# Kernel tuning notes

Hardware: AMD Instinct MI355X
Metric: run time of the kernel (lower is better)

Reference implementation:

```python
import jax, jax.numpy as jnp
import numpy as np

B, N, C = 2, 2048, 1024
H = 16
D = C // H  # head_dim = 64
HID = 4 * C
EPS = 1e-5


def _layernorm(x, g, b):
    mu = jnp.mean(x, axis=-1, keepdims=True)
    var = jnp.var(x, axis=-1, keepdims=True)
    return (x - mu) * jax.lax.rsqrt(var + EPS) * g + b


def _rope(x):
    # x: (B, H, N, D); interleaved-pair rotation, sin/cos computed in fp32
    half = D // 2
    inv_freq = 1.0 / (10000.0 ** (jnp.arange(half, dtype=jnp.float32) / half))
    pos = jnp.arange(N, dtype=jnp.float32)
    freqs = pos[:, None] * inv_freq[None, :]            # (N, half)
    sin = jnp.sin(freqs).astype(x.dtype)
    cos = jnp.cos(freqs).astype(x.dtype)
    xr = x.reshape(*x.shape[:-1], half, 2)
    x1, x2 = xr[..., 0], xr[..., 1]
    r1 = x1 * cos - x2 * sin
    r2 = x1 * sin + x2 * cos
    return jnp.stack((r1, r2), axis=-1).reshape(x.shape)


def setup_inputs() -> dict:
    key = jax.random.key(0)
    ks = jax.random.split(key, 8)
    s = lambda d: 1.0 / np.sqrt(d)
    return {
        "x": jax.random.normal(ks[0], (B, N, C), jnp.float32),
        "ln1_g": jnp.ones((C,), jnp.float32),
        "ln1_b": jnp.zeros((C,), jnp.float32),
        "W_qkv": jax.random.normal(ks[1], (C, 3 * C), jnp.float32) * s(C),
        "b_qkv": jnp.zeros((3 * C,), jnp.float32),
        "W_proj": jax.random.normal(ks[2], (C, C), jnp.float32) * s(C),
        "b_proj": jnp.zeros((C,), jnp.float32),
        "ln2_g": jnp.ones((C,), jnp.float32),
        "ln2_b": jnp.zeros((C,), jnp.float32),
        "W_fc1": jax.random.normal(ks[3], (C, HID), jnp.float32) * s(C),
        "b_fc1": jnp.zeros((HID,), jnp.float32),
        "W_fc2": jax.random.normal(ks[4], (HID, C), jnp.float32) * s(HID),
        "b_fc2": jnp.zeros((C,), jnp.float32),
    }


def reference(x, ln1_g, ln1_b, W_qkv, b_qkv, W_proj, b_proj,
              ln2_g, ln2_b, W_fc1, b_fc1, W_fc2, b_fc2):
    # --- attention branch ---
    h = _layernorm(x, ln1_g, ln1_b)
    qkv = h @ W_qkv + b_qkv                              # (B, N, 3C)
    qkv = qkv.reshape(B, N, 3, H, D).transpose(2, 0, 3, 1, 4)
    q, k, v = qkv[0], qkv[1], qkv[2]                     # each (B, H, N, D)
    q = _rope(q)
    k = _rope(k)
    scale = D ** -0.5
    attn = jnp.einsum('bhnd,bhmd->bhnm', q, k) * scale
    attn = jax.nn.softmax(attn, axis=-1)
    o = jnp.einsum('bhnm,bhmd->bhnd', attn, v)           # (B, H, N, D)
    o = o.transpose(0, 2, 1, 3).reshape(B, N, C)
    x = x + (o @ W_proj + b_proj)
    # --- MLP branch ---
    h = _layernorm(x, ln2_g, ln2_b)
    h = jax.nn.gelu(h @ W_fc1 + b_fc1, approximate=False)
    x = x + (h @ W_fc2 + b_fc2)
    return x
```

## Files before the change

### kernel.cpp

```cpp
#include <hip/hip_runtime.h>
#include <cstdint>
#include <cstddef>

typedef unsigned short u16;
typedef unsigned int   u32;
typedef __attribute__((ext_vector_type(8))) short v8s;
typedef __attribute__((ext_vector_type(4))) float v4f;

#define B_   2
#define N_   2048
#define C_   1024
#define H_   16
#define D_   64
#define HID_ 4096
#define M_   4096

static __device__ __forceinline__ float b2f(u32 u) {
    union { u32 i; float f; } x; x.i = u << 16; return x.f;
}
static __device__ __forceinline__ u16 f2b(float f) {
    union { float f; u32 i; } x; x.f = f;
    u32 r = (x.i + 0x7fffu + ((x.i >> 16) & 1u)) >> 16;
    return (u16)r;
}
static __device__ __forceinline__ u32 scale2(u32 raw, float s) {
    float lo = b2f(raw & 0xffffu) * s, hi = b2f(raw >> 16) * s;
    return (u32)f2b(lo) | ((u32)f2b(hi) << 16);
}

static __device__ __forceinline__ void gload_lds16(const u16* g, u16* l) {
    __builtin_amdgcn_global_load_lds(
        (const __attribute__((address_space(1))) void*)g,
        (__attribute__((address_space(3))) void*)l,
        16, 0, 0);
}

static __device__ __forceinline__ int2 xcd_swz(int gx, int gy) {
    const int nwg = gx * gy;
    int id = blockIdx.y * gx + blockIdx.x;
    id = (id & 7) * (nwg >> 3) + (id >> 3);
    return make_int2(id % gx, id / gx);
}

__global__ __launch_bounds__(256) void transpose_all(const float* __restrict__ Wqkv,
                                                     const float* __restrict__ Wproj,
                                                     const float* __restrict__ Wfc1,
                                                     const float* __restrict__ Wfc2,
                                                     u16* __restrict__ Oqkv,
                                                     u16* __restrict__ Oproj,
                                                     u16* __restrict__ Ofc1,
                                                     u16* __restrict__ Ofc2) {
    __shared__ float tile[32][33];
    int id = blockIdx.x;
    const float* in; u16* out; int K, N, nx;
    if (id < 3072)      { in = Wqkv;  out = Oqkv;  K = 1024; N = 3072; nx = 96;  }
    else if (id < 4096) { in = Wproj; out = Oproj; K = 1024; N = 1024; nx = 32;  id -= 3072; }
    else if (id < 8192) { in = Wfc1;  out = Ofc1;  K = 1024; N = 4096; nx = 128; id -= 4096; }
    else                { in = Wfc2;  out = Ofc2;  K = 4096; N = 1024; nx = 32;  id -= 8192; }
    const int n0 = (id % nx) * 32, k0 = (id / nx) * 32;
    const int c = threadIdx.x & 31, r8 = threadIdx.x >> 5;
#pragma unroll
    for (int i = 0; i < 4; ++i)
        tile[r8 + i * 8][c] = in[(size_t)(k0 + r8 + i * 8) * N + n0 + c];
    __syncthreads();
#pragma unroll
    for (int i = 0; i < 4; ++i)
        out[(size_t)(n0 + r8 + i * 8) * K + k0 + c] = f2b(tile[c][r8 + i * 8]);
}

__global__ __launch_bounds__(256) void ln_kernel(const float* __restrict__ in,
                                                 const float* __restrict__ g,
                                                 const float* __restrict__ b,
                                                 u16* __restrict__ out) {
    __shared__ float ps[4], psq[4];
    __shared__ float stats[2];
    const int row = blockIdx.x;
    const int t = threadIdx.x;
    float4 v = ((const float4*)in)[(size_t)row * 256 + t];
    float s  = v.x + v.y + v.z + v.w;
    float sq = v.x * v.x + v.y * v.y + v.z * v.z + v.w * v.w;
#pragma unroll
    for (int off = 32; off > 0; off >>= 1) { s += __shfl_down(s, off); sq += __shfl_down(sq, off); }
    if ((t & 63) == 0) { ps[t >> 6] = s; psq[t >> 6] = sq; }
    __syncthreads();
    if (t == 0) {
        float S = ps[0] + ps[1] + ps[2] + ps[3];
        float Q = psq[0] + psq[1] + psq[2] + psq[3];
        float mu  = S * (1.f / 1024.f);
        float var = Q * (1.f / 1024.f) - mu * mu;
        stats[0] = mu; stats[1] = rsqrtf(var + 1e-5f);
    }
    __syncthreads();
    const float mu = stats[0], istd = stats[1];
    float4 gg = ((const float4*)g)[t];
    float4 bb = ((const float4*)b)[t];
    ushort4 o;
    o.x = f2b((v.x - mu) * istd * gg.x + bb.x);
    o.y = f2b((v.y - mu) * istd * gg.y + bb.y);
    o.z = f2b((v.z - mu) * istd * gg.z + bb.z);
    o.w = f2b((v.w - mu) * istd * gg.w + bb.w);
    *(ushort4*)&out[(size_t)row * 1024 + t * 4] = o;
}

__global__ __launch_bounds__(256) void rope_table(float2* __restrict__ tab) {
    const int i = blockIdx.x * 256 + threadIdx.x;
    const int d = i & 31, n = i >> 5;
    float inv = powf(10000.f, -(float)d * (1.f / 32.f));
    float fr = (float)n * inv;
    tab[i] = make_float2(cosf(fr), sinf(fr));
}

template <int EPI, int BM>
__global__ __launch_bounds__(256) void gemm_bt(const u16* __restrict__ A,
                                               const u16* __restrict__ Bt,
                                               const float* __restrict__ bias,
                                               void* __restrict__ outp,
                                               const float* __restrict__ resid,
                                               const float2* __restrict__ tab,
                                               int Ndim, int Kdim) {
    constexpr int NACC = (BM == 128) ? 4 : 2;
    constexpr int AISS = BM / 64;
    __shared__ u16 As[3][BM * 32];
    __shared__ u16 Bs[3][128 * 32];
    const int t = threadIdx.x;
    const int lane = t & 63;
    const int w = t >> 6;
    const int wr = (BM == 128) ? (w >> 1) : 0;
    const int wc = (BM == 128) ? (w & 1) : w;
    const int2 lb = xcd_swz(gridDim.x, gridDim.y);
    const int m0 = lb.y * BM, n0 = lb.x * 128;
    const int hi = lane >> 4, lo = lane & 15;

    auto STAGE = [&](int buf, int kt) {
#pragma unroll
        for (int j = 0; j < AISS; ++j) {
            const int c = (w * AISS + j) * 64 + lane;
            gload_lds16(&A[(size_t)(m0 + (c >> 2)) * Kdim + kt + (c & 3) * 8],
                        &As[buf][(w * AISS + j) * 512]);
        }
#pragma unroll
        for (int j = 0; j < 2; ++j) {
            const int c = (w * 2 + j) * 64 + lane;
            gload_lds16(&Bt[(size_t)(n0 + (c >> 2)) * Kdim + kt + (c & 3) * 8],
                        &Bs[buf][(w * 2 + j) * 512]);
        }
    };

    const v4f vzero = {0.f, 0.f, 0.f, 0.f};
    v4f acc[4][NACC];
#pragma unroll
    for (int i = 0; i < 4; ++i)
#pragma unroll
        for (int j = 0; j < NACC; ++j) acc[i][j] = vzero;

    const int nt = Kdim / 32;
    STAGE(0, 0);
    STAGE(1, 32);
    for (int kt = 0; kt < nt; ++kt) {
        if constexpr (BM == 128) asm volatile("s_waitcnt vmcnt(4)" ::: "memory");
        else                     asm volatile("s_waitcnt vmcnt(3)" ::: "memory");
        __builtin_amdgcn_s_barrier();
        if (kt + 2 < nt) STAGE((kt + 2) % 3, (kt + 2) * 32);
        const int cur = kt % 3;
        v8s av[4], bv[NACC];
#pragma unroll
        for (int mi = 0; mi < 4; ++mi)
            av[mi] = *(const v8s*)&As[cur][(wr * 64 + mi * 16 + lo) * 32 + hi * 8];
#pragma unroll
        for (int ni = 0; ni < NACC; ++ni)
            bv[ni] = *(const v8s*)&Bs[cur][(wc * (NACC * 16) + ni * 16 + lo) * 32 + hi * 8];
#pragma unroll
        for (int mi = 0; mi < 4; ++mi)
#pragma unroll
            for (int ni = 0; ni < NACC; ++ni)
                acc[mi][ni] = __builtin_amdgcn_mfma_f32_16x16x32_bf16(av[mi], bv[ni], acc[mi][ni], 0, 0, 0);
    }

#pragma unroll
    for (int mi = 0; mi < 4; ++mi)
#pragma unroll
        for (int ni = 0; ni < NACC; ++ni) {
            const int col = n0 + wc * (NACC * 16) + ni * 16 + lo;
            const float bsv = bias[col];
#pragma unroll
            for (int r = 0; r < 4; ++r) {
                const int row = m0 + wr * 64 + mi * 16 + hi * 4 + r;
                float vacc = acc[mi][ni][r] + bsv;
                if (EPI == 0) {
                    const float partner = __shfl_xor(vacc, 1);
                    const int s = col >> 10;
                    if (s < 2) {
                        const int d = col & 63;
                        const int n = row & 2047;
                        float2 cs = tab[n * 32 + (d >> 1)];
                        vacc = vacc * cs.x + ((d & 1) ? partner * cs.y : -partner * cs.y);
                    }
                    const int rem = col & 1023, hh = rem >> 6, dd = rem & 63;
                    const int bb = row >> 11, nn = row & 2047;
                    ((u16*)outp)[((((size_t)s * B_ + bb) * H_ + hh) * N_ + nn) * D_ + dd] = f2b(vacc);
                } else if (EPI == 1) {
                    ((float*)outp)[(size_t)row * Ndim + col] = vacc + resid[(size_t)row * Ndim + col];
                } else {
                    const float gv = 0.5f * vacc * (1.f + erff(vacc * 0.70710678118f));
                    ((u16*)outp)[(size_t)row * Ndim + col] = f2b(gv);
                }
            }
        }
}

#define SCL_LOG2E 0.1803368801111244f
#define FIXEDM    12.0f

__global__ __launch_bounds__(256) void attn_mfma(const u16* __restrict__ q,
                                                 const u16* __restrict__ k,
                                                 const u16* __restrict__ v,
                                                 u16* __restrict__ out) {
    __shared__ u16 Ks[64 * 64];
    __shared__ u16 Vt[64 * 64];
    __shared__ u16 Ps[4][32 * 64];

    const int t    = threadIdx.x;
    const int w    = t >> 6;
    const int lane = t & 63;
    const int hi   = lane >> 4;
    const int lo   = lane & 15;
    const int2 lb  = xcd_swz(gridDim.x, gridDim.y);
    const int bh   = lb.y;
    const int r0g  = lb.x * 128 + w * 32;

    const u16* qb = q + (size_t)bh * N_ * D_;
    const u16* kb = k + (size_t)bh * N_ * D_;
    const u16* vb = v + (size_t)bh * N_ * D_;

    v8s qa[2][2];
#pragma unroll
    for (int mi = 0; mi < 2; ++mi)
#pragma unroll
        for (int ks = 0; ks < 2; ++ks) {
            uint4 rq = *(const uint4*)&qb[(size_t)(r0g + mi * 16 + lo) * 64 + ks * 32 + hi * 8];
            u32 qs[4];
            qs[0] = scale2(rq.x, SCL_LOG2E); qs[1] = scale2(rq.y, SCL_LOG2E);
            qs[2] = scale2(rq.z, SCL_LOG2E); qs[3] = scale2(rq.w, SCL_LOG2E);
            qa[mi][ks] = *(v8s*)qs;
        }

    u32 ones4[4] = {0x3F803F80u, 0x3F803F80u, 0x3F803F80u, 0x3F803F80u};
    const v8s ones = *(v8s*)ones4;

    const v4f vzero = {0.f, 0.f, 0.f, 0.f};
    v4f o_acc[2][4];
    v4f l_acc[2];
#pragma unroll
    for (int mi = 0; mi < 2; ++mi) {
        l_acc[mi] = vzero;
#pragma unroll
        for (int ni = 0; ni < 4; ++ni) o_acc[mi][ni] = vzero;
    }

    const int vp = t & 31, vg = t >> 5;
    const int vd0 = vg * 8, vkey = vp * 2;

    for (int kt = 0; kt < N_ / 64; ++kt) {
        __syncthreads();
#pragma unroll
        for (int i = 0; i < 2; ++i) {
            const int chunk = i * 256 + t;
            const int key = chunk >> 3, d0 = (chunk & 7) * 8;
            uint4 raw = *(const uint4*)&kb[(size_t)(kt * 64 + key) * 64 + d0];
            *(uint4*)&Ks[key * 64 + (d0 ^ ((key & 7) << 3))] = raw;
        }
        {
            uint4 r0 = *(const uint4*)&vb[(size_t)(kt * 64 + vkey) * 64 + vd0];
            uint4 r1 = *(const uint4*)&vb[(size_t)(kt * 64 + vkey + 1) * 64 + vd0];
            const u32* a0 = (const u32*)&r0;
            const u32* a1 = (const u32*)&r1;
#pragma unroll
            for (int j = 0; j < 8; ++j) {
                u32 lo16 = (j & 1) ? (a0[j >> 1] >> 16) : (a0[j >> 1] & 0xffffu);
                u32 hi16 = (j & 1) ? (a1[j >> 1] >> 16) : (a1[j >> 1] & 0xffffu);
                u32 val = lo16 | (hi16 << 16);
                *(u32*)&Vt[(vd0 + j) * 64 + (vkey ^ (j << 3))] = val;
            }
        }
        __syncthreads();

        v4f s[2][4];
#pragma unroll
        for (int mi = 0; mi < 2; ++mi)
#pragma unroll
            for (int ni = 0; ni < 4; ++ni) s[mi][ni] = vzero;
        __builtin_amdgcn_s_setprio(1);
#pragma unroll
        for (int ks = 0; ks < 2; ++ks)
#pragma unroll
            for (int ni = 0; ni < 4; ++ni) {
                const int key = lo + 16 * ni;
                v8s bv = *(const v8s*)&Ks[key * 64 + ((ks * 32 + hi * 8) ^ ((key & 7) << 3))];
                s[0][ni] = __builtin_amdgcn_mfma_f32_16x16x32_bf16(qa[0][ks], bv, s[0][ni], 0, 0, 0);
                s[1][ni] = __builtin_amdgcn_mfma_f32_16x16x32_bf16(qa[1][ks], bv, s[1][ni], 0, 0, 0);
            }
        __builtin_amdgcn_s_setprio(0);

#pragma unroll
        for (int mi = 0; mi < 2; ++mi)
#pragma unroll
            for (int ni = 0; ni < 4; ++ni)
#pragma unroll
                for (int r = 0; r < 4; ++r)
                    s[mi][ni][r] = exp2f(s[mi][ni][r] - FIXEDM);

#pragma unroll
        for (int mi = 0; mi < 2; ++mi)
#pragma unroll
            for (int f = 0; f < 4; ++f)
#pragma unroll
                for (int rp = 0; rp < 2; ++rp) {
                    u32 pk;
                    asm("v_cvt_pk_bf16_f32 %0, %1, %2"
                        : "=v"(pk) : "v"(s[mi][f][2 * rp]), "v"(s[mi][f][2 * rp + 1]));
                    const int row0 = mi * 16 + hi * 4 + 2 * rp;
                    const int row1 = row0 + 1;
                    Ps[w][row0 * 64 + ((lo + 16 * f) ^ ((row0 & 7) << 3))] = (u16)pk;
                    Ps[w][row1 * 64 + ((lo + 16 * f) ^ ((row1 & 7) << 3))] = (u16)(pk >> 16);
                }
        v8s pa[2][2];
#pragma unroll
        for (int mi = 0; mi < 2; ++mi)
#pragma unroll
            for (int ks = 0; ks < 2; ++ks) {
                const int row = mi * 16 + lo;
                pa[mi][ks] = *(const v8s*)&Ps[w][row * 64 + ((ks * 32 + hi * 8) ^ ((lo & 7) << 3))];
            }

        __builtin_amdgcn_s_setprio(1);
#pragma unroll
        for (int ks = 0; ks < 2; ++ks) {
#pragma unroll
            for (int ni = 0; ni < 4; ++ni) {
                const int dim = lo + 16 * ni;
                v8s vv = *(const v8s*)&Vt[dim * 64 + ((ks * 32 + hi * 8) ^ ((dim & 7) << 3))];
                o_acc[0][ni] = __builtin_amdgcn_mfma_f32_16x16x32_bf16(pa[0][ks], vv, o_acc[0][ni], 0, 0, 0);
                o_acc[1][ni] = __builtin_amdgcn_mfma_f32_16x16x32_bf16(pa[1][ks], vv, o_acc[1][ni], 0, 0, 0);
            }
            l_acc[0] = __builtin_amdgcn_mfma_f32_16x16x32_bf16(pa[0][ks], ones, l_acc[0], 0, 0, 0);
            l_acc[1] = __builtin_amdgcn_mfma_f32_16x16x32_bf16(pa[1][ks], ones, l_acc[1], 0, 0, 0);
        }
        __builtin_amdgcn_s_setprio(0);
    }

    const int bb = bh >> 4, hh = bh & 15;
#pragma unroll
    for (int mi = 0; mi < 2; ++mi)
#pragma unroll
        for (int r = 0; r < 4; ++r) {
            const float inv = 1.f / l_acc[mi][r];
            const int n = r0g + mi * 16 + hi * 4 + r;
#pragma unroll
            for (int ni = 0; ni < 4; ++ni) {
                out[((size_t)bb * N_ + n) * C_ + hh * D_ + lo + 16 * ni] = f2b(o_acc[mi][ni][r] * inv);
            }
        }
}

extern "C" void kernel_launch(void* const* d_in, const int* in_sizes, int n_in,
                              void* d_out, int out_size, void* d_ws, size_t ws_size,
                              hipStream_t stream) {
    (void)in_sizes; (void)n_in; (void)out_size; (void)ws_size;
    const float* x     = (const float*)d_in[0];
    const float* ln1g  = (const float*)d_in[1];
    const float* ln1b  = (const float*)d_in[2];
    const float* Wqkv  = (const float*)d_in[3];
    const float* bqkv  = (const float*)d_in[4];
    const float* Wproj = (const float*)d_in[5];
    const float* bproj = (const float*)d_in[6];
    const float* ln2g  = (const float*)d_in[7];
    const float* ln2b  = (const float*)d_in[8];
    const float* Wfc1  = (const float*)d_in[9];
    const float* bfc1  = (const float*)d_in[10];
    const float* Wfc2  = (const float*)d_in[11];
    const float* bfc2  = (const float*)d_in[12];
    float* out = (float*)d_out;

    char* base = (char*)d_ws;
    const size_t MB = 1024 * 1024;
    u16* Wtqkv  = (u16*)(base);
    u16* Wtproj = (u16*)(base + 6 * MB);
    u16* Wtfc1  = (u16*)(base + 8 * MB);
    u16* Wtfc2  = (u16*)(base + 16 * MB);
    u16* qkv    = (u16*)(base + 24 * MB);
    u16* a1     = (u16*)(base + 24 * MB);
    u16* h1     = (u16*)(base + 56 * MB);
    u16* oatt   = (u16*)(base + 56 * MB);
    u16* h2     = (u16*)(base + 56 * MB);
    float* x1   = (float*)(base + 64 * MB);
    float2* tab = (float2*)(base + 80 * MB);

    transpose_all<<<12288, 256, 0, stream>>>(Wqkv, Wproj, Wfc1, Wfc2,
                                             Wtqkv, Wtproj, Wtfc1, Wtfc2);
    rope_table<<<N_ * (D_ / 2) / 256, 256, 0, stream>>>(tab);
    ln_kernel<<<M_, 256, 0, stream>>>(x, ln1g, ln1b, h1);
    gemm_bt<0, 128><<<dim3(3 * C_ / 128, M_ / 128), 256, 0, stream>>>(h1, Wtqkv, bqkv, qkv, nullptr, tab, 3 * C_, C_);
    attn_mfma<<<dim3(N_ / 128, B_ * H_), 256, 0, stream>>>(
        qkv, qkv + (size_t)B_ * H_ * N_ * D_, qkv + (size_t)2 * B_ * H_ * N_ * D_, oatt);
    gemm_bt<1, 64><<<dim3(C_ / 128, M_ / 64), 256, 0, stream>>>(oatt, Wtproj, bproj, x1, x, nullptr, C_, C_);
    ln_kernel<<<M_, 256, 0, stream>>>(x1, ln2g, ln2b, h2);
    gemm_bt<2, 128><<<dim3(HID_ / 128, M_ / 128), 256, 0, stream>>>(h2, Wtfc1, bfc1, a1, nullptr, nullptr, HID_, C_);
    gemm_bt<1, 64><<<dim3(C_ / 128, M_ / 64), 256, 0, stream>>>(a1, Wtfc2, bfc2, out, x1, nullptr, C_, HID_);
}
```

Before: 304.1 us.

## Split attention over two key halves with a separate combine kernel

The attention kernel now splits the key sequence into two halves across a doubled grid. Each block writes unnormalized fp32 partial outputs and row sums to workspace, and a new combine kernel adds them and normalizes to bf16. This relies on the fixed-max softmax, which needs no rescaling between halves. The aim is to raise block count and occupancy for attention (512 to 1024 blocks on a large-CU GPU). The cost is extra fp32 global traffic of about 32MB written and read, plus one more kernel launch.

```diff
diff --git a/kernel.cpp b/kernel.cpp
--- a/kernel.cpp
+++ b/kernel.cpp
@@ -214,7 +214,8 @@
 __global__ __launch_bounds__(256) void attn_mfma(const u16* __restrict__ q,
                                                  const u16* __restrict__ k,
                                                  const u16* __restrict__ v,
-                                                 u16* __restrict__ out) {
+                                                 float* __restrict__ opart,
+                                                 float* __restrict__ lpart) {
     __shared__ u16 Ks[64 * 64];
     __shared__ u16 Vt[64 * 64];
     __shared__ u16 Ps[4][32 * 64];
@@ -225,7 +226,8 @@
     const int hi   = lane >> 4;
     const int lo   = lane & 15;
     const int2 lb  = xcd_swz(gridDim.x, gridDim.y);
-    const int bh   = lb.y;
+    const int bh   = lb.y >> 1;
+    const int split = lb.y & 1;
     const int r0g  = lb.x * 128 + w * 32;
 
     const u16* qb = q + (size_t)bh * N_ * D_;
@@ -260,7 +262,8 @@
     const int vp = t & 31, vg = t >> 5;
     const int vd0 = vg * 8, vkey = vp * 2;
 
-    for (int kt = 0; kt < N_ / 64; ++kt) {
+    const int kt0 = split * (N_ / 128);
+    for (int kt = kt0; kt < kt0 + N_ / 128; ++kt) {
         __syncthreads();
 #pragma unroll
         for (int i = 0; i < 2; ++i) {
@@ -353,13 +356,39 @@
     for (int mi = 0; mi < 2; ++mi)
 #pragma unroll
         for (int r = 0; r < 4; ++r) {
-            const float inv = 1.f / l_acc[mi][r];
             const int n = r0g + mi * 16 + hi * 4 + r;
+            if (lo == 0)
+                lpart[((size_t)split * (B_ * H_) + bh) * N_ + n] = l_acc[mi][r];
 #pragma unroll
             for (int ni = 0; ni < 4; ++ni) {
-                out[((size_t)bb * N_ + n) * C_ + hh * D_ + lo + 16 * ni] = f2b(o_acc[mi][ni][r] * inv);
-            }
-        }
+                opart[((size_t)(split * B_ + bb) * N_ + n) * C_ + hh * D_ + lo + 16 * ni] =
+                    o_acc[mi][ni][r];
+            }
+        }
+}
+
+__global__ __launch_bounds__(256) void attn_combine(const float* __restrict__ opart,
+                                                    const float* __restrict__ lpart,
+                                                    u16* __restrict__ out) {
+    const int row = blockIdx.x;
+    const int bb = row >> 11, n = row & 2047;
+    const int t = threadIdx.x;
+    const int c0 = t * 4;
+    const int hh = c0 >> 6;
+    const int bh = bb * H_ + hh;
+    const float l0 = lpart[(size_t)bh * N_ + n];
+    const float l1 = lpart[((size_t)(B_ * H_) + bh) * N_ + n];
+    const float inv = 1.f / (l0 + l1);
+    const size_t off0 = ((size_t)bb * N_ + n) * C_ + c0;
+    const size_t off1 = ((size_t)(B_ + bb) * N_ + n) * C_ + c0;
+    float4 a = *(const float4*)&opart[off0];
+    float4 b4 = *(const float4*)&opart[off1];
+    ushort4 o;
+    o.x = f2b((a.x + b4.x) * inv);
+    o.y = f2b((a.y + b4.y) * inv);
+    o.z = f2b((a.z + b4.z) * inv);
+    o.w = f2b((a.w + b4.w) * inv);
+    *(ushort4*)&out[((size_t)bb * N_ + n) * C_ + c0] = o;
 }
 
 extern "C" void kernel_launch(void* const* d_in, const int* in_sizes, int n_in,
@@ -394,14 +423,17 @@
     u16* h2     = (u16*)(base + 56 * MB);
     float* x1   = (float*)(base + 64 * MB);
     float2* tab = (float2*)(base + 80 * MB);
+    float* opart = (float*)(base + 81 * MB);
+    float* lpart = (float*)(base + 113 * MB);
 
     transpose_all<<<12288, 256, 0, stream>>>(Wqkv, Wproj, Wfc1, Wfc2,
                                              Wtqkv, Wtproj, Wtfc1, Wtfc2);
     rope_table<<<N_ * (D_ / 2) / 256, 256, 0, stream>>>(tab);
     ln_kernel<<<M_, 256, 0, stream>>>(x, ln1g, ln1b, h1);
     gemm_bt<0, 128><<<dim3(3 * C_ / 128, M_ / 128), 256, 0, stream>>>(h1, Wtqkv, bqkv, qkv, nullptr, tab, 3 * C_, C_);
-    attn_mfma<<<dim3(N_ / 128, B_ * H_), 256, 0, stream>>>(
-        qkv, qkv + (size_t)B_ * H_ * N_ * D_, qkv + (size_t)2 * B_ * H_ * N_ * D_, oatt);
+    attn_mfma<<<dim3(N_ / 128, 2 * B_ * H_), 256, 0, stream>>>(
+        qkv, qkv + (size_t)B_ * H_ * N_ * D_, qkv + (size_t)2 * B_ * H_ * N_ * D_, opart, lpart);
+    attn_combine<<<M_, 256, 0, stream>>>(opart, lpart, oatt);
     gemm_bt<1, 64><<<dim3(C_ / 128, M_ / 64), 256, 0, stream>>>(oatt, Wtproj, bproj, x1, x, nullptr, C_, C_);
     ln_kernel<<<M_, 256, 0, stream>>>(x1, ln2g, ln2b, h2);
     gemm_bt<2, 128><<<dim3(HID_ / 128, M_ / 128), 256, 0, stream>>>(h2, Wtfc1, bfc1, a1, nullptr, nullptr, HID_, C_);
```

New measurement: 313.2 us. 3.0% more time.

## Add 256x256-tile 8-wave GEMM with interleaved prefetch for FC1+GELU

Applied to the files above, without the earlier changes.

Replaces the 128x128 FC1 GEMM with a new 512-thread kernel that computes 256x256 output tiles, double-buffering LDS in k-halves and interleaving async global-to-LDS prefetch between MFMA groups with priority raises. Larger tiles raise arithmetic intensity and cut redundant global reads of A and B. The trade-offs are a 16x16 grid of only 256 blocks, which may leave CUs underused, heavy register pressure from 32 accumulators per lane, and a manual vmcnt/barrier schedule that must be exactly right.

```diff
diff --git a/kernel.cpp b/kernel.cpp
--- a/kernel.cpp
+++ b/kernel.cpp
@@ -208,6 +208,121 @@
         }
 }
 
+__global__ __launch_bounds__(512, 2) void gemm256_gelu(const u16* __restrict__ A,
+                                                       const u16* __restrict__ Bt,
+                                                       const float* __restrict__ bias,
+                                                       u16* __restrict__ outp,
+                                                       int Ndim, int Kdim) {
+    __shared__ u16 As[2 * 2 * 256 * 32];
+    __shared__ u16 Bs[2 * 2 * 256 * 32];
+    const int t = threadIdx.x;
+    const int lane = t & 63;
+    const int w = t >> 6;
+    const int wr = w >> 2, wc = w & 3;
+    const int hi = lane >> 4, lo = lane & 15;
+    const int2 lb = xcd_swz(gridDim.x, gridDim.y);
+    const int m0 = lb.y * 256, n0 = lb.x * 256;
+    const int koff = (hi * 8) ^ ((lo & 2) << 3);
+
+    auto STAGEH = [&](u16* lds, const u16* src, int rb, int b, int ks, int kt) {
+#pragma unroll
+        for (int j = 0; j < 2; ++j) {
+            const int c = j * 512 + t;
+            const int row = c >> 2;
+            const int e0 = (c & 3) * 8;
+            gload_lds16(&src[(size_t)(rb + row) * Kdim + kt * 64 + ks * 32 + (e0 ^ ((row & 2) << 3))],
+                        &lds[(b * 2 + ks) * 8192 + c * 8]);
+        }
+    };
+    auto RD = [&](const u16* lds, int b, int ks, int row) -> v8s {
+        return *(const v8s*)&lds[(b * 2 + ks) * 8192 + row * 32 + koff];
+    };
+
+    const v4f vzero = {0.f, 0.f, 0.f, 0.f};
+    v4f acc[8][4];
+#pragma unroll
+    for (int i = 0; i < 8; ++i)
+#pragma unroll
+        for (int j = 0; j < 4; ++j) acc[i][j] = vzero;
+
+    const int nt = Kdim / 64;
+    STAGEH(As, A, m0, 0, 0, 0);
+    STAGEH(Bs, Bt, n0, 0, 0, 0);
+    STAGEH(As, A, m0, 0, 1, 0);
+    STAGEH(Bs, Bt, n0, 0, 1, 0);
+
+    for (int I = 0; I < nt; ++I) {
+        const int b = I & 1, nb = b ^ 1;
+        const bool pf = (I + 1 < nt);
+        v8s av[4], bv[4];
+        asm volatile("s_waitcnt vmcnt(4)" ::: "memory");
+        __builtin_amdgcn_s_barrier();
+#pragma unroll
+        for (int n = 0; n < 4; ++n) bv[n] = RD(Bs, b, 0, wc * 64 + n * 16 + lo);
+#pragma unroll
+        for (int m = 0; m < 4; ++m) av[m] = RD(As, b, 0, wr * 128 + m * 16 + lo);
+        if (pf) STAGEH(As, A, m0, nb, 0, I + 1);
+        __builtin_amdgcn_s_setprio(1);
+#pragma unroll
+        for (int m = 0; m < 4; ++m)
+#pragma unroll
+            for (int n = 0; n < 4; ++n)
+                acc[m][n] = __builtin_amdgcn_mfma_f32_16x16x32_bf16(av[m], bv[n], acc[m][n], 0, 0, 0);
+        __builtin_amdgcn_s_setprio(0);
+        __builtin_amdgcn_s_barrier();
+#pragma unroll
+        for (int m = 0; m < 4; ++m) av[m] = RD(As, b, 0, wr * 128 + 64 + m * 16 + lo);
+        if (pf) STAGEH(Bs, Bt, n0, nb, 0, I + 1);
+        __builtin_amdgcn_s_setprio(1);
+#pragma unroll
+        for (int m = 0; m < 4; ++m)
+#pragma unroll
+            for (int n = 0; n < 4; ++n)
+                acc[4 + m][n] = __builtin_amdgcn_mfma_f32_16x16x32_bf16(av[m], bv[n], acc[4 + m][n], 0, 0, 0);
+        __builtin_amdgcn_s_setprio(0);
+        asm volatile("s_waitcnt vmcnt(4)" ::: "memory");
+        __builtin_amdgcn_s_barrier();
+#pragma unroll
+        for (int n = 0; n < 4; ++n) bv[n] = RD(Bs, b, 1, wc * 64 + n * 16 + lo);
+#pragma unroll
+        for (int m = 0; m < 4; ++m) av[m] = RD(As, b, 1, wr * 128 + m * 16 + lo);
+        if (pf) STAGEH(As, A, m0, nb, 1, I + 1);
+        __builtin_amdgcn_s_setprio(1);
+#pragma unroll
+        for (int m = 0; m < 4; ++m)
+#pragma unroll
+            for (int n = 0; n < 4; ++n)
+                acc[m][n] = __builtin_amdgcn_mfma_f32_16x16x32_bf16(av[m], bv[n], acc[m][n], 0, 0, 0);
+        __builtin_amdgcn_s_setprio(0);
+        __builtin_amdgcn_s_barrier();
+#pragma unroll
+        for (int m = 0; m < 4; ++m) av[m] = RD(As, b, 1, wr * 128 + 64 + m * 16 + lo);
+        if (pf) STAGEH(Bs, Bt, n0, nb, 1, I + 1);
+        __builtin_amdgcn_s_setprio(1);
+#pragma unroll
+        for (int m = 0; m < 4; ++m)
+#pragma unroll
+            for (int n = 0; n < 4; ++n)
+                acc[4 + m][n] = __builtin_amdgcn_mfma_f32_16x16x32_bf16(av[m], bv[n], acc[4 + m][n], 0, 0, 0);
+        __builtin_amdgcn_s_setprio(0);
+    }
+
+#pragma unroll
+    for (int mi = 0; mi < 8; ++mi)
+#pragma unroll
+        for (int ni = 0; ni < 4; ++ni) {
+            const int col = n0 + wc * 64 + ni * 16 + lo;
+            const float bsv = bias[col];
+#pragma unroll
+            for (int r = 0; r < 4; ++r) {
+                const int row = m0 + wr * 128 + mi * 16 + hi * 4 + r;
+                float vacc = acc[mi][ni][r] + bsv;
+                const float gv = 0.5f * vacc * (1.f + erff(vacc * 0.70710678118f));
+                outp[(size_t)row * Ndim + col] = f2b(gv);
+            }
+        }
+}
+
 #define SCL_LOG2E 0.1803368801111244f
 #define FIXEDM    12.0f
 
@@ -404,6 +519,6 @@
         qkv, qkv + (size_t)B_ * H_ * N_ * D_, qkv + (size_t)2 * B_ * H_ * N_ * D_, oatt);
     gemm_bt<1, 64><<<dim3(C_ / 128, M_ / 64), 256, 0, stream>>>(oatt, Wtproj, bproj, x1, x, nullptr, C_, C_);
     ln_kernel<<<M_, 256, 0, stream>>>(x1, ln2g, ln2b, h2);
-    gemm_bt<2, 128><<<dim3(HID_ / 128, M_ / 128), 256, 0, stream>>>(h2, Wtfc1, bfc1, a1, nullptr, nullptr, HID_, C_);
+    gemm256_gelu<<<dim3(HID_ / 256, M_ / 256), 512, 0, stream>>>(h2, Wtfc1, bfc1, a1, HID_, C_);
     gemm_bt<1, 64><<<dim3(C_ / 128, M_ / 64), 256, 0, stream>>>(a1, Wtfc2, bfc2, out, x1, nullptr, C_, HID_);
 }
```

Result: faster. 288.7 us (-5.0%).
